# Performance work log

Hardware: AMD Instinct MI355X
Metric: run time of the kernel (lower is better)

The kernel has to match this reference:

```python
import jax, jax.numpy as jnp
import numpy as np

CDF = 0.9  # sparse_threshold


def setup_inputs() -> dict:
    key = jax.random.key(0)
    ks = jax.random.split(key, 8)
    BS, FPS, PPF, XC, K, YS = 8, 64, 1024, 64, 64, 128
    N = BS * FPS * PPF  # 524288 points
    x = jax.random.normal(ks[0], (N, XC), jnp.float32)
    # locations: cols 0,1 are spatial coords, col 2 is the (sorted) frame id;
    # uniform ragged structure: exactly PPF points per frame.
    frame_id = (jnp.arange(N, dtype=jnp.int32) // PPF)
    loc01 = jax.random.randint(ks[1], (N, 2), 0, 64, dtype=jnp.int32)
    locations = jnp.concatenate([loc01, frame_id[:, None]], axis=1)
    y = jax.random.normal(ks[2], (BS, YS), jnp.float32)
    Wc = jax.random.normal(ks[3], (K, XC), jnp.float32) * 0.05
    bc = jnp.zeros((K,), jnp.float32)
    Wy = jax.random.normal(ks[4], (K, YS), jnp.float32) * 0.05
    Wa = jax.random.normal(ks[5], (1, K), jnp.float32) * 0.05
    ba = jnp.zeros((1,), jnp.float32)
    return {"x": x, "locations": locations, "y": y, "Wc": Wc, "bc": bc,
            "Wy": Wy, "Wa": Wa, "ba": ba,
            "frames_per_sample": FPS, "points_per_frame": PPF}


def reference(x, locations, y, Wc, bc, Wy, Wa, ba, frames_per_sample, points_per_frame):
    N, XC = x.shape
    P = points_per_frame
    T = N // P                       # total frames = sum(x_lens)
    y_k = y @ Wy.T                   # [bs, k]   (y_affine, no bias)
    x_k = x @ Wc.T + bc              # [N, k]    (channel_affine)
    frame_id = locations[:, 2]       # [N]
    batch_id = frame_id // frames_per_sample  # which sample each point belongs to
    # attn_weight_affine(tanh(x_k + y_k[sample]))  -> [N]
    scores = (jnp.tanh(x_k + y_k[batch_id]) @ Wa.T + ba)[:, 0]
    w = jax.nn.softmax(scores.reshape(T, P), axis=-1)  # per-frame softmax
    # top-p (CDF) sparsification per frame: sort desc, cumsum < cdf, keep one more
    order = jnp.argsort(-w, axis=-1)                      # [T, P] desc order
    w_sorted = jnp.take_along_axis(w, order, axis=-1)
    csum = jnp.cumsum(w_sorted, axis=-1)
    keep = jnp.sum(csum < CDF, axis=-1) + 1               # mask[sum(mask)] = True
    rank = jnp.argsort(order, axis=-1)                    # inverse permutation
    mask = (rank < keep[:, None]).reshape(-1)             # [N] bool
    new_x = x[mask, :]
    new_locations = locations[mask, :]
    return new_x, new_locations
```

## Files before the change

### kernel.cpp

```cpp
#include <hip/hip_runtime.h>
#include <math.h>


typedef __attribute__((ext_vector_type(8))) short short8v;
typedef __attribute__((ext_vector_type(4))) float f32x4;

__device__ __forceinline__ unsigned short bf16rne(float f) {
    unsigned u = __builtin_bit_cast(unsigned, f);
    return (unsigned short)((u + 0x7fffu + ((u >> 16) & 1u)) >> 16);
}
__device__ __forceinline__ float bf16f(unsigned short h) {
    unsigned u = ((unsigned)h) << 16;
    return __builtin_bit_cast(float, u);
}

__device__ __forceinline__ float fast_tanh(float z) {
    float az = fabsf(z);
    float e  = __expf(-2.0f * az);
    float r  = (1.0f - e) * __builtin_amdgcn_rcpf(1.0f + e);
    return copysignf(r, z);
}

__global__ __launch_bounds__(512) void yk_kernel(const float* __restrict__ y,
                                                 const float* __restrict__ Wy,
                                                 float* __restrict__ yk) {
    const int tid = threadIdx.x;
    const int b = tid >> 6, k = tid & 63;
    const float* yrow = y + b * 128;
    const float* wrow = Wy + k * 128;
    float a0 = 0.f, a1 = 0.f, a2 = 0.f, a3 = 0.f;
#pragma unroll
    for (int j = 0; j < 128; j += 4) {
        a0 += yrow[j + 0] * wrow[j + 0];
        a1 += yrow[j + 1] * wrow[j + 1];
        a2 += yrow[j + 2] * wrow[j + 2];
        a3 += yrow[j + 3] * wrow[j + 3];
    }
    yk[tid] = (a0 + a1) + (a2 + a3);
}

__global__ __launch_bounds__(256) void wsplit_kernel(const float* __restrict__ Wc,
                                                     const float* __restrict__ bc,
                                                     const float* __restrict__ Wa,
                                                     const float* __restrict__ yk,
                                                     short8v* __restrict__ wfrag,
                                                     float* __restrict__ pre,
                                                     float* __restrict__ waCopy) {
    const int tid = threadIdx.x;
    for (int f = tid; f < 1536; f += 256) {
        int ln = f & 63, t = f >> 6, kt = t & 3, pc = t >> 2;
        int cs = pc & 1, pr = pc >> 1;
        int k = kt * 16 + (ln & 15), c = cs * 32 + 8 * (ln >> 4);
        const float* wr = Wc + k * 64 + c;
        short8v o;
#pragma unroll
        for (int j = 0; j < 8; ++j) {
            float v = wr[j];
            unsigned short hb = bf16rne(v);
            if (pr == 0) { o[j] = (short)hb; continue; }
            float r1 = v - bf16f(hb);
            unsigned short mb = bf16rne(r1);
            if (pr == 1) { o[j] = (short)mb; continue; }
            float r2 = r1 - bf16f(mb);
            o[j] = (short)bf16rne(r2);
        }
        wfrag[f] = o;
    }
    for (int p = tid; p < 512; p += 256) pre[p] = bc[p & 63] + yk[p];
    if (tid < 64) waCopy[tid] = Wa[tid];
}

__global__ __launch_bounds__(256, 4) void score_kernel(const float* __restrict__ x,
                                                       const short8v* __restrict__ wfrag,
                                                       const float* __restrict__ pre,
                                                       const float* __restrict__ waCopy,
                                                       const float* __restrict__ ba,
                                                       float* __restrict__ scores) {
    __shared__ short8v sWf[1536];
    __shared__ float sPre[64];
    __shared__ float sWaS[64];
    const int tid  = threadIdx.x;
    const int lane = tid & 63;
    const int wv   = tid >> 6;
    const int b    = blockIdx.x >> 9;
    const int pbase = blockIdx.x * 128 + wv * 32;

    const int prow0 = pbase + (lane & 15);
    const int cg = 8 * (lane >> 4);
    float4 u[2][2][2];
#pragma unroll
    for (int pt = 0; pt < 2; ++pt) {
        const float* xr = x + (long long)(prow0 + pt * 16) * 64;
#pragma unroll
        for (int cs = 0; cs < 2; ++cs) {
            const float4* xp4 = (const float4*)(xr + cs * 32 + cg);
            u[pt][cs][0] = xp4[0];
            u[pt][cs][1] = xp4[1];
        }
    }

    for (int f = tid; f < 1536; f += 256) sWf[f] = wfrag[f];
    if (tid < 64) { sPre[tid] = pre[b * 64 + tid]; sWaS[tid] = waCopy[tid]; }
    __syncthreads();

    short8v A[2][3][2];
#pragma unroll
    for (int pt = 0; pt < 2; ++pt) {
#pragma unroll
        for (int cs = 0; cs < 2; ++cs) {
            float4 u0 = u[pt][cs][0], u1 = u[pt][cs][1];
            float v[8] = {u0.x, u0.y, u0.z, u0.w, u1.x, u1.y, u1.z, u1.w};
            short8v h, m, l;
#pragma unroll
            for (int j = 0; j < 8; ++j) {
                float vv = v[j];
                unsigned short hb = bf16rne(vv);
                float r1 = vv - bf16f(hb);
                unsigned short mb = bf16rne(r1);
                float r2 = r1 - bf16f(mb);
                h[j] = (short)hb; m[j] = (short)mb; l[j] = (short)bf16rne(r2);
            }
            A[pt][0][cs] = h; A[pt][1][cs] = m; A[pt][2][cs] = l;
        }
    }

    f32x4 sacc[2] = {{0.f, 0.f, 0.f, 0.f}, {0.f, 0.f, 0.f, 0.f}};
    const float ba0 = ba[0];
    const int kcol = lane & 15;
#pragma unroll
    for (int kt = 0; kt < 4; ++kt) {
        short8v B[3][2];
#pragma unroll
        for (int pr = 0; pr < 3; ++pr)
#pragma unroll
            for (int cs = 0; cs < 2; ++cs)
                B[pr][cs] = sWf[((pr * 2 + cs) * 4 + kt) * 64 + lane];
        const float prek = sPre[kt * 16 + kcol];
        const float wak = sWaS[kt * 16 + kcol];
#pragma unroll
        for (int pt = 0; pt < 2; ++pt) {
            f32x4 acc = {0.f, 0.f, 0.f, 0.f};
#pragma unroll
            for (int cs = 0; cs < 2; ++cs) {
                acc = __builtin_amdgcn_mfma_f32_16x16x32_bf16(A[pt][2][cs], B[0][cs], acc, 0, 0, 0);
                acc = __builtin_amdgcn_mfma_f32_16x16x32_bf16(A[pt][0][cs], B[2][cs], acc, 0, 0, 0);
                acc = __builtin_amdgcn_mfma_f32_16x16x32_bf16(A[pt][1][cs], B[1][cs], acc, 0, 0, 0);
                acc = __builtin_amdgcn_mfma_f32_16x16x32_bf16(A[pt][1][cs], B[0][cs], acc, 0, 0, 0);
                acc = __builtin_amdgcn_mfma_f32_16x16x32_bf16(A[pt][0][cs], B[1][cs], acc, 0, 0, 0);
                acc = __builtin_amdgcn_mfma_f32_16x16x32_bf16(A[pt][0][cs], B[0][cs], acc, 0, 0, 0);
            }
#pragma unroll
            for (int r = 0; r < 4; ++r) {
                float z = acc[r] + prek;
                sacc[pt][r] += wak * fast_tanh(z);
            }
        }
    }

#pragma unroll
    for (int pt = 0; pt < 2; ++pt)
#pragma unroll
        for (int r = 0; r < 4; ++r) {
            float v = sacc[pt][r];
            v += __shfl_xor(v, 1);
            v += __shfl_xor(v, 2);
            v += __shfl_xor(v, 4);
            v += __shfl_xor(v, 8);
            if (kcol == 0)
                scores[pbase + pt * 16 + (lane >> 4) * 4 + r] = v + ba0;
        }
}

__global__ __launch_bounds__(1024) void tile_kernel(const float* __restrict__ scores,
                                                    int* __restrict__ flags,
                                                    int* __restrict__ keepcnt) {
    const int t = blockIdx.x, tid = threadIdx.x;
    __shared__ float sw[1024];
    __shared__ int   si[1024];
    __shared__ float red[16];
    __shared__ int   keep_s;

    const int lane = tid & 63, wid = tid >> 6;
    float s = scores[t * 1024 + tid];

    float m = s;
#pragma unroll
    for (int o = 32; o; o >>= 1) m = fmaxf(m, __shfl_xor(m, o));
    if (lane == 0) red[wid] = m;
    __syncthreads();
    float mb = red[0];
#pragma unroll
    for (int q = 1; q < 16; ++q) mb = fmaxf(mb, red[q]);
    __syncthreads();

    float e = expf(s - mb);
    float su = e;
#pragma unroll
    for (int o = 32; o; o >>= 1) su += __shfl_xor(su, o);
    if (lane == 0) red[wid] = su;
    __syncthreads();
    float tot = 0.f;
#pragma unroll
    for (int q = 0; q < 16; ++q) tot += red[q];

    float w  = e / tot;
    int   idx = tid;

    for (int kk = 2; kk <= 1024; kk <<= 1) {
        for (int j = kk >> 1; j > 0; j >>= 1) {
            bool lower = (tid & j) == 0;
            bool desc2 = (tid & kk) == 0;
            float wp; int ip;
            if (j >= 64) {
                sw[tid] = w; si[tid] = idx;
                __syncthreads();
                wp = sw[tid ^ j]; ip = si[tid ^ j];
                bool before = (w > wp) || (w == wp && idx < ip);
                bool keep = desc2 ? (before == lower) : (before != lower);
                if (!keep) { w = wp; idx = ip; }
                __syncthreads();
            } else {
                wp = __shfl_xor(w, j);
                ip = __shfl_xor(idx, j);
                bool before = (w > wp) || (w == wp && idx < ip);
                bool keep = desc2 ? (before == lower) : (before != lower);
                if (!keep) { w = wp; idx = ip; }
            }
        }
    }

    sw[tid] = w;
    __syncthreads();

    if (tid == 0) {
        float c = 0.f; int kp = 0;
#pragma unroll 8
        for (int q = 0; q < 1024; ++q) { c += sw[q]; if (c < 0.9f) ++kp; }
        keep_s = kp + 1;
        keepcnt[t] = kp + 1;
    }
    __syncthreads();

    flags[t * 1024 + idx] = (tid < keep_s) ? 1 : 0;
}

__global__ __launch_bounds__(64) void offsets_kernel(const int* __restrict__ keepcnt,
                                                     int* __restrict__ toffs, int T) {
    const int lane = threadIdx.x;
    const int base = lane * 8;
    int v[8]; int s = 0;
#pragma unroll
    for (int j = 0; j < 8; ++j) { v[j] = keepcnt[base + j]; s += v[j]; }
    int inc = s;
#pragma unroll
    for (int o = 1; o < 64; o <<= 1) {
        int tmp = __shfl_up(inc, o);
        if (lane >= o) inc += tmp;
    }
    int r = inc - s;
#pragma unroll
    for (int j = 0; j < 8; ++j) { toffs[base + j] = r; r += v[j]; }
}

__global__ __launch_bounds__(1024) void compact_kernel(const float* __restrict__ x,
                                                       const int* __restrict__ locs,
                                                       const int* __restrict__ flags,
                                                       const int* __restrict__ toffs,
                                                       float* __restrict__ out,
                                                       int M) {
    const int t = blockIdx.x, tid = threadIdx.x;
    const long long gi = (long long)t * 1024 + tid;
    const int f = flags[gi];
    const int lane = tid & 63, wid = tid >> 6;

    unsigned long long ball = __ballot(f != 0);
    int wpre = __popcll(ball & (((unsigned long long)1 << lane) - 1ULL));

    __shared__ int wtot[16];
    __shared__ int woff[16];
    if (lane == 63) wtot[wid] = wpre + f;
    __syncthreads();
    if (tid == 0) {
        int r = 0;
#pragma unroll
        for (int q = 0; q < 16; ++q) { woff[q] = r; r += wtot[q]; }
    }
    __syncthreads();

    if (f) {
        const long long pos = (long long)toffs[t] + woff[wid] + wpre;
        const float4* src = (const float4*)(x + gi * 64);
        float4* dst = (float4*)(out + pos * 64);
#pragma unroll
        for (int j = 0; j < 16; ++j) dst[j] = src[j];
        float* lout = out + (long long)M * 64 + pos * 3;
        lout[0] = (float)locs[gi * 3 + 0];
        lout[1] = (float)locs[gi * 3 + 1];
        lout[2] = (float)locs[gi * 3 + 2];
    }
}

extern "C" void kernel_launch(void* const* d_in, const int* in_sizes, int n_in,
                              void* d_out, int out_size, void* d_ws, size_t ws_size,
                              hipStream_t stream) {
    const float* x    = (const float*)d_in[0];
    const int*   locs = (const int*)d_in[1];
    const float* y    = (const float*)d_in[2];
    const float* Wc   = (const float*)d_in[3];
    const float* bc   = (const float*)d_in[4];
    const float* Wy   = (const float*)d_in[5];
    const float* Wa   = (const float*)d_in[6];
    const float* ba   = (const float*)d_in[7];

    const int N = in_sizes[0] / 64;
    const int T = N / 1024;
    const int M = out_size / 67;

    float* ws      = (float*)d_ws;
    float* yk      = ws;
    float* scores  = ws + 512;
    int*   flags   = (int*)(ws + 512 + N);
    int*   keepcnt = flags + N;
    int*   toffs   = keepcnt + T;
    short8v* wfrag = (short8v*)(ws + 512 + 2 * N + 2 * T);
    float* pre     = ws + 512 + 2 * N + 2 * T + 6144;
    float* waCopy  = pre + 512;

    yk_kernel<<<1, 512, 0, stream>>>(y, Wy, yk);
    wsplit_kernel<<<1, 256, 0, stream>>>(Wc, bc, Wa, yk, wfrag, pre, waCopy);
    score_kernel<<<N / 128, 256, 0, stream>>>(x, wfrag, pre, waCopy, ba, scores);
    tile_kernel<<<T, 1024, 0, stream>>>(scores, flags, keepcnt);
    offsets_kernel<<<1, 64, 0, stream>>>(keepcnt, toffs, T);
    compact_kernel<<<T, 1024, 0, stream>>>(x, locs, flags, toffs, (float*)d_out, M);
}
```

Baseline: 161.4 us.

## Fuse prep kernels, truncate bf16 split, and coalesce compaction row copies

Merges the y-projection and weight-split kernels into one prep kernel, removing a launch and a global round trip. The activation three-way bf16 split in the score kernel now truncates instead of rounding to nearest, which is cheaper per element; the residual chain should still carry most of the lost bits. The compaction kernel records source rows for kept points in shared memory and copies them with 16 threads per row, giving contiguous 256-byte accesses instead of one thread streaming a whole row. This adds extra barriers and a loop in the compaction step.

Measured after the change: 134.2 us. -16.8%, faster.

```diff
diff --git a/kernel.cpp b/kernel.cpp
--- a/kernel.cpp
+++ b/kernel.cpp
@@ -21,33 +21,33 @@
     return copysignf(r, z);
 }
 
-__global__ __launch_bounds__(512) void yk_kernel(const float* __restrict__ y,
-                                                 const float* __restrict__ Wy,
-                                                 float* __restrict__ yk) {
+__global__ __launch_bounds__(512) void prep_kernel(const float* __restrict__ y,
+                                                   const float* __restrict__ Wy,
+                                                   const float* __restrict__ Wc,
+                                                   const float* __restrict__ bc,
+                                                   const float* __restrict__ Wa,
+                                                   short8v* __restrict__ wfrag,
+                                                   float* __restrict__ pre,
+                                                   float* __restrict__ waCopy) {
+    __shared__ float yks[512];
     const int tid = threadIdx.x;
-    const int b = tid >> 6, k = tid & 63;
-    const float* yrow = y + b * 128;
-    const float* wrow = Wy + k * 128;
-    float a0 = 0.f, a1 = 0.f, a2 = 0.f, a3 = 0.f;
-#pragma unroll
-    for (int j = 0; j < 128; j += 4) {
-        a0 += yrow[j + 0] * wrow[j + 0];
-        a1 += yrow[j + 1] * wrow[j + 1];
-        a2 += yrow[j + 2] * wrow[j + 2];
-        a3 += yrow[j + 3] * wrow[j + 3];
-    }
-    yk[tid] = (a0 + a1) + (a2 + a3);
-}
-
-__global__ __launch_bounds__(256) void wsplit_kernel(const float* __restrict__ Wc,
-                                                     const float* __restrict__ bc,
-                                                     const float* __restrict__ Wa,
-                                                     const float* __restrict__ yk,
-                                                     short8v* __restrict__ wfrag,
-                                                     float* __restrict__ pre,
-                                                     float* __restrict__ waCopy) {
-    const int tid = threadIdx.x;
-    for (int f = tid; f < 1536; f += 256) {
+    {
+        const int b = tid >> 6, k = tid & 63;
+        const float* yrow = y + b * 128;
+        const float* wrow = Wy + k * 128;
+        float a0 = 0.f, a1 = 0.f, a2 = 0.f, a3 = 0.f;
+#pragma unroll
+        for (int j = 0; j < 128; j += 4) {
+            a0 += yrow[j + 0] * wrow[j + 0];
+            a1 += yrow[j + 1] * wrow[j + 1];
+            a2 += yrow[j + 2] * wrow[j + 2];
+            a3 += yrow[j + 3] * wrow[j + 3];
+        }
+        yks[tid] = (a0 + a1) + (a2 + a3);
+    }
+    __syncthreads();
+
+    for (int f = tid; f < 1536; f += 512) {
         int ln = f & 63, t = f >> 6, kt = t & 3, pc = t >> 2;
         int cs = pc & 1, pr = pc >> 1;
         int k = kt * 16 + (ln & 15), c = cs * 32 + 8 * (ln >> 4);
@@ -66,7 +66,7 @@
         }
         wfrag[f] = o;
     }
-    for (int p = tid; p < 512; p += 256) pre[p] = bc[p & 63] + yk[p];
+    pre[tid] = bc[tid & 63] + yks[tid];
     if (tid < 64) waCopy[tid] = Wa[tid];
 }
 
@@ -114,11 +114,12 @@
 #pragma unroll
             for (int j = 0; j < 8; ++j) {
                 float vv = v[j];
-                unsigned short hb = bf16rne(vv);
+                unsigned short hb = (unsigned short)(__builtin_bit_cast(unsigned, vv) >> 16);
                 float r1 = vv - bf16f(hb);
-                unsigned short mb = bf16rne(r1);
+                unsigned short mb = (unsigned short)(__builtin_bit_cast(unsigned, r1) >> 16);
                 float r2 = r1 - bf16f(mb);
-                h[j] = (short)hb; m[j] = (short)mb; l[j] = (short)bf16rne(r2);
+                unsigned short lb = (unsigned short)(__builtin_bit_cast(unsigned, r2) >> 16);
+                h[j] = (short)hb; m[j] = (short)mb; l[j] = (short)lb;
             }
             A[pt][0][cs] = h; A[pt][1][cs] = m; A[pt][2][cs] = l;
         }
@@ -278,25 +279,41 @@
 
     __shared__ int wtot[16];
     __shared__ int woff[16];
+    __shared__ int rowsrc[1024];
+    __shared__ int nk_s;
     if (lane == 63) wtot[wid] = wpre + f;
     __syncthreads();
     if (tid == 0) {
         int r = 0;
 #pragma unroll
         for (int q = 0; q < 16; ++q) { woff[q] = r; r += wtot[q]; }
-    }
-    __syncthreads();
-
+        nk_s = r;
+    }
+    __syncthreads();
+
+    const int base = toffs[t];
     if (f) {
-        const long long pos = (long long)toffs[t] + woff[wid] + wpre;
-        const float4* src = (const float4*)(x + gi * 64);
-        float4* dst = (float4*)(out + pos * 64);
-#pragma unroll
-        for (int j = 0; j < 16; ++j) dst[j] = src[j];
+        const int local = woff[wid] + wpre;
+        rowsrc[local] = tid;
+        const long long pos = (long long)base + local;
         float* lout = out + (long long)M * 64 + pos * 3;
         lout[0] = (float)locs[gi * 3 + 0];
         lout[1] = (float)locs[gi * 3 + 1];
         lout[2] = (float)locs[gi * 3 + 2];
+    }
+    __syncthreads();
+
+    const int nk = nk_s;
+    const int rsub = tid >> 4;
+    const int col  = tid & 15;
+    for (int r0 = 0; r0 < nk; r0 += 64) {
+        const int rr = r0 + rsub;
+        if (rr < nk) {
+            const int srow = rowsrc[rr];
+            const float4* src = (const float4*)(x + ((long long)t * 1024 + srow) * 64);
+            float4* dst = (float4*)(out + (long long)(base + rr) * 64);
+            dst[col] = src[col];
+        }
     }
 }
 
@@ -317,7 +334,6 @@
     const int M = out_size / 67;
 
     float* ws      = (float*)d_ws;
-    float* yk      = ws;
     float* scores  = ws + 512;
     int*   flags   = (int*)(ws + 512 + N);
     int*   keepcnt = flags + N;
@@ -326,8 +342,7 @@
     float* pre     = ws + 512 + 2 * N + 2 * T + 6144;
     float* waCopy  = pre + 512;
 
-    yk_kernel<<<1, 512, 0, stream>>>(y, Wy, yk);
-    wsplit_kernel<<<1, 256, 0, stream>>>(Wc, bc, Wa, yk, wfrag, pre, waCopy);
+    prep_kernel<<<1, 512, 0, stream>>>(y, Wy, Wc, bc, Wa, wfrag, pre, waCopy);
     score_kernel<<<N / 128, 256, 0, stream>>>(x, wfrag, pre, waCopy, ba, scores);
     tile_kernel<<<T, 1024, 0, stream>>>(scores, flags, keepcnt);
     offsets_kernel<<<1, 64, 0, stream>>>(keepcnt, toffs, T);
```
